# Performance work log

Hardware: AMD Instinct MI355X
Metric: run time of the kernel (lower is better)

The kernel has to match this reference:

```python
import jax, jax.numpy as jnp
import numpy as np

# Config constants (match init_kwargs / config)
B = 16        # config.BATCH_SIZE
T = 2048      # config.TRAIN_LEN
C = 256       # input channels (input_shape[-1])
K = 8         # kernel_size
F = 256       # nb_filters
DIL = 4       # dilation_rate


def setup_inputs() -> dict:
    key = jax.random.key(0)
    k1, k2, k3 = jax.random.split(key, 3)
    inputs = jax.random.normal(k1, (B, T, C), dtype=jnp.float32)
    kernel = jax.random.normal(k2, (C, K, F), dtype=jnp.float32) * 0.05
    bias = jax.random.normal(k3, (F,), dtype=jnp.float32) * 0.05
    return {"inputs": inputs, "kernel": kernel, "bias": bias}


def reference(inputs, kernel, bias):
    # Original TF layer computes, per (b,t,k,f):
    #   raw[b,t,k,f] = sum_c (x[b,t,c] * kernel[c,k,f] + bias[f])
    #               = conv[b,t,k,f] + C * bias[f]
    # (bias is added BEFORE the reduce_sum over the channel axis, so it is
    #  scaled by C — we reproduce that quirk faithfully.)
    # Then each (t,k) slice is scatter-added to output time t + k*dilation
    # (the gather_nd + zero-pad construction in TF implements exactly this
    #  dilated transposed-conv scatter; non-matching positions gather zeros),
    # and finally the last T timesteps are kept.
    Bq, Tq, Cq = inputs.shape
    Kq, Fq = kernel.shape[1], kernel.shape[2]
    conv = jnp.einsum('btc,ckf->btkf', inputs, kernel) + jnp.asarray(Cq, inputs.dtype) * bias
    L = Tq + (Kq - 1) * DIL  # final_time_len
    # scatter positions: out[i + j*DIL] += conv[:, i, j, :]
    pos = (jnp.arange(Tq)[:, None] + DIL * jnp.arange(Kq)[None, :]).reshape(-1)  # (T*K,)
    out = jnp.zeros((Bq, L, Fq), dtype=conv.dtype)
    out = out.at[:, pos, :].add(conv.reshape(Bq, Tq * Kq, Fq))
    return out[:, -Tq:, :]
```

## Files before the change

kernel.cpp:

```cpp
#include <hip/hip_runtime.h>
#include <hip/hip_bf16.h>


#define B_    16
#define T_    2048
#define C_    256
#define KT    8
#define F_    256
#define SH    28
#define BT    128
#define ROWS  (BT + SH)
#define NTASK (ROWS * 8)
#define CHW   (ROWS * 64)

typedef __attribute__((ext_vector_type(8))) short short8;
typedef __attribute__((ext_vector_type(4))) float floatx4;

__global__ __launch_bounds__(256) void wprep_kernel(const float* __restrict__ W,
                                                    ushort* __restrict__ Wf) {
    const int tid  = threadIdx.x;
    const int fid  = blockIdx.x * 4 + (tid >> 6);
    const int lane = tid & 63;
    const int g    = fid & 15;
    const int S    = fid >> 4;
    const int kh   = S & 1, j = (S >> 1) & 7, cs = S >> 4;
    const int c0   = cs * 64 + kh * 32 + (lane >> 4) * 8;
    const int f    = g * 16 + (lane & 15);
    short8 pk;
    #pragma unroll
    for (int i = 0; i < 8; ++i) {
        __hip_bfloat16 h = __float2bfloat16(W[((c0 + i) * KT + j) * F_ + f]);
        pk[i] = *reinterpret_cast<const short*>(&h);
    }
    *reinterpret_cast<short8*>(Wf + (size_t)fid * 512 + lane * 8) = pk;
}

__device__ inline short8 cvt8(float4 a, float4 b) {
    float v[8] = {a.x, a.y, a.z, a.w, b.x, b.y, b.z, b.w};
    short8 r;
    #pragma unroll
    for (int i = 0; i < 8; ++i) {
        __hip_bfloat16 h = __float2bfloat16(v[i]);
        r[i] = *reinterpret_cast<const short*>(&h);
    }
    return r;
}

__global__ __launch_bounds__(512, 2) void deconv_kernel(
        const float* __restrict__ x, const ushort* __restrict__ Wf,
        const float* __restrict__ bias, float* __restrict__ out) {
    __shared__ ushort xs[2 * CHW];
    const int t0   = blockIdx.x * BT;
    const int b    = blockIdx.y;
    const int tid  = threadIdx.x;
    const int lane = tid & 63, w = tid >> 6;
    const int wf   = w & 3, wm = w >> 2;
    const int l16  = lane & 15, q = lane >> 4;

    const int r0 = tid >> 3,          g0 = tid & 7;
    const int r1 = (tid + 512) >> 3,  g1 = tid & 7;
    const int r2 = (tid + 1024) >> 3, g2 = tid & 7;

    float4 A0, B0, A1, B1, A2, B2;

#define STAGE_LOAD(cs_) do {                                                   \
        const float4 z_ = make_float4(0.f, 0.f, 0.f, 0.f);                     \
        A0 = z_; B0 = z_; A1 = z_; B1 = z_; A2 = z_; B2 = z_;                  \
        {   const float4* p_ = reinterpret_cast<const float4*>(                \
                x + ((size_t)(b * T_ + t0 + r0) * C_ + (cs_) * 64 + g0 * 8));  \
            A0 = p_[0]; B0 = p_[1]; }                                          \
        {   const float4* p_ = reinterpret_cast<const float4*>(                \
                x + ((size_t)(b * T_ + t0 + r1) * C_ + (cs_) * 64 + g1 * 8));  \
            A1 = p_[0]; B1 = p_[1]; }                                          \
        if (tid < 224 && t0 + r2 < T_) {                                       \
            const float4* p_ = reinterpret_cast<const float4*>(                \
                x + ((size_t)(b * T_ + t0 + r2) * C_ + (cs_) * 64 + g2 * 8));  \
            A2 = p_[0]; B2 = p_[1]; } } while (0)

#define STAGE_WRITE(buf_) do {                                                 \
        ushort* d_ = xs + (buf_) * CHW;                                        \
        *reinterpret_cast<short8*>(d_ + r0 * 64 + ((g0 ^ (r0 & 7)) * 8)) =     \
            cvt8(A0, B0);                                                      \
        *reinterpret_cast<short8*>(d_ + r1 * 64 + ((g1 ^ (r1 & 7)) * 8)) =     \
            cvt8(A1, B1);                                                      \
        if (tid < 224)                                                         \
            *reinterpret_cast<short8*>(d_ + r2 * 64 + ((g2 ^ (r2 & 7)) * 8)) = \
                cvt8(A2, B2);                                                  \
        } while (0)

#define LOAD_A(buf_, s_, arr) do {                                             \
        const int j_ = (s_) >> 1, kh_ = (s_) & 1;                              \
        const int rb_ = SH - 4 * j_ + wm * 64 + l16;                           \
        _Pragma("unroll")                                                      \
        for (int mf = 0; mf < 4; ++mf) {                                       \
            const int row_ = rb_ + mf * 16;                                    \
            arr[mf] = *reinterpret_cast<const short8*>(                        \
                xs + (buf_) * CHW + row_ * 64 +                                \
                (((kh_ * 4 + q) ^ (row_ & 7)) * 8));                           \
        } } while (0)

#define LOAD_B(S_, arr) do {                                                   \
        const ushort* p_ = wbase + (size_t)(S_) * 8192;                        \
        _Pragma("unroll")                                                      \
        for (int nf = 0; nf < 4; ++nf)                                         \
            arr[nf] = *reinterpret_cast<const short8*>(p_ + nf * 512);         \
        } while (0)

#define DO_MFMA(aa, bb) do {                                                   \
        _Pragma("unroll")                                                      \
        for (int mf = 0; mf < 4; ++mf)                                         \
            _Pragma("unroll")                                                  \
            for (int nf = 0; nf < 4; ++nf)                                     \
                acc[mf][nf] = __builtin_amdgcn_mfma_f32_16x16x32_bf16(         \
                    aa[mf], bb[nf], acc[mf][nf], 0, 0, 0);                     \
        } while (0)

    const ushort* wbase = Wf + wf * 2048 + (size_t)lane * 8;

    float bf4[4];
    #pragma unroll
    for (int nf = 0; nf < 4; ++nf) bf4[nf] = bias[wf * 64 + nf * 16 + l16];

    floatx4 acc[4][4];
    #pragma unroll
    for (int mf = 0; mf < 4; ++mf)
        #pragma unroll
        for (int nf = 0; nf < 4; ++nf)
            acc[mf][nf] = (floatx4){0.f, 0.f, 0.f, 0.f};

    short8 aA[4], aB[4], bA[4], bB[4];

    STAGE_LOAD(0);
    LOAD_B(0, bA);
    LOAD_B(1, bB);
    STAGE_WRITE(0);
    __syncthreads();

    for (int cs = 0; cs < 4; ++cs) {
        const int buf = cs & 1;
        if (cs < 3) STAGE_LOAD(cs + 1);
        LOAD_A(buf, 0, aA);
        LOAD_A(buf, 1, aB);
        #pragma unroll
        for (int s = 0; s < 16; s += 2) {
            const int S = cs * 16 + s;
            __builtin_amdgcn_s_setprio(1);
            DO_MFMA(aA, bA);
            __builtin_amdgcn_s_setprio(0);
            if (s < 14) LOAD_A(buf, s + 2, aA);
            LOAD_B((S + 2) & 63, bA);
            __builtin_amdgcn_s_setprio(1);
            DO_MFMA(aB, bB);
            __builtin_amdgcn_s_setprio(0);
            if (s < 14) LOAD_A(buf, s + 3, aB);
            LOAD_B((S + 3) & 63, bB);
        }
        if (cs < 3) STAGE_WRITE(buf ^ 1);
        __syncthreads();
    }

    #pragma unroll
    for (int mf = 0; mf < 4; ++mf) {
        #pragma unroll
        for (int nf = 0; nf < 4; ++nf) {
            const int f = wf * 64 + nf * 16 + l16;
            #pragma unroll
            for (int r = 0; r < 4; ++r) {
                const int t = t0 + wm * 64 + mf * 16 + q * 4 + r;
                const int jmin = (t < T_ - SH) ? 0 : (((t - (T_ - SH)) >> 2) + 1);
                out[(size_t)(b * T_ + t) * F_ + f] =
                    acc[mf][nf][r] + (float)(8 - jmin) * 256.0f * bf4[nf];
            }
        }
    }
#undef STAGE_LOAD
#undef STAGE_WRITE
#undef LOAD_A
#undef LOAD_B
#undef DO_MFMA
}

extern "C" void kernel_launch(void* const* d_in, const int* in_sizes, int n_in,
                              void* d_out, int out_size, void* d_ws, size_t ws_size,
                              hipStream_t stream) {
    const float* x    = (const float*)d_in[0];
    const float* W    = (const float*)d_in[1];
    const float* bias = (const float*)d_in[2];
    float* out = (float*)d_out;
    ushort* Wf = (ushort*)d_ws;

    wprep_kernel<<<256, 256, 0, stream>>>(W, Wf);
    dim3 grid(T_ / BT, B_);
    deconv_kernel<<<grid, 512, 0, stream>>>(x, Wf, bias, out);
}
```

Baseline: 45.23 us.

## Switch deconv to 32x32x16 MFMA with 4 waves and 32-channel stages

```diff
diff --git a/kernel.cpp b/kernel.cpp
--- a/kernel.cpp
+++ b/kernel.cpp
@@ -10,27 +10,28 @@
 #define SH    28
 #define BT    128
 #define ROWS  (BT + SH)
-#define NTASK (ROWS * 8)
-#define CHW   (ROWS * 64)
+#define CH    32
+#define CHW   (ROWS * CH)
 
 typedef __attribute__((ext_vector_type(8))) short short8;
-typedef __attribute__((ext_vector_type(4))) float floatx4;
+typedef __attribute__((ext_vector_type(16))) float floatx16;
 
 __global__ __launch_bounds__(256) void wprep_kernel(const float* __restrict__ W,
                                                     ushort* __restrict__ Wf) {
     const int tid  = threadIdx.x;
     const int fid  = blockIdx.x * 4 + (tid >> 6);
     const int lane = tid & 63;
-    const int g    = fid & 15;
-    const int S    = fid >> 4;
-    const int kh   = S & 1, j = (S >> 1) & 7, cs = S >> 4;
-    const int c0   = cs * 64 + kh * 32 + (lane >> 4) * 8;
-    const int f    = g * 16 + (lane & 15);
+    const int l5 = lane & 31, h = lane >> 5;
+    const int nf = fid & 1, w = (fid >> 1) & 3;
+    const int S  = fid >> 3;
+    const int kh = S & 1, j = (S >> 1) & 7, cs = S >> 4;
+    const int c0 = cs * 32 + kh * 16 + h * 8;
+    const int f  = w * 64 + nf * 32 + l5;
     short8 pk;
     #pragma unroll
     for (int i = 0; i < 8; ++i) {
-        __hip_bfloat16 h = __float2bfloat16(W[((c0 + i) * KT + j) * F_ + f]);
-        pk[i] = *reinterpret_cast<const short*>(&h);
+        __hip_bfloat16 v = __float2bfloat16(W[((c0 + i) * KT + j) * F_ + f]);
+        pk[i] = *reinterpret_cast<const short*>(&v);
     }
     *reinterpret_cast<short8*>(Wf + (size_t)fid * 512 + lane * 8) = pk;
 }
@@ -40,13 +41,13 @@
     short8 r;
     #pragma unroll
     for (int i = 0; i < 8; ++i) {
-        __hip_bfloat16 h = __float2bfloat16(v[i]);
-        r[i] = *reinterpret_cast<const short*>(&h);
+        __hip_bfloat16 t = __float2bfloat16(v[i]);
+        r[i] = *reinterpret_cast<const short*>(&t);
     }
     return r;
 }
 
-__global__ __launch_bounds__(512, 2) void deconv_kernel(
+__global__ __launch_bounds__(256, 1) void deconv_kernel(
         const float* __restrict__ x, const ushort* __restrict__ Wf,
         const float* __restrict__ bias, float* __restrict__ out) {
     __shared__ ushort xs[2 * CHW];
@@ -54,81 +55,79 @@
     const int b    = blockIdx.y;
     const int tid  = threadIdx.x;
     const int lane = tid & 63, w = tid >> 6;
-    const int wf   = w & 3, wm = w >> 2;
-    const int l16  = lane & 15, q = lane >> 4;
+    const int l5   = lane & 31, h = lane >> 5;
 
-    const int r0 = tid >> 3,          g0 = tid & 7;
-    const int r1 = (tid + 512) >> 3,  g1 = tid & 7;
-    const int r2 = (tid + 1024) >> 3, g2 = tid & 7;
+    const int r0 = tid >> 2,            g0 = tid & 3;
+    const int r1 = (tid + 256) >> 2,    g1 = tid & 3;
+    const int r2 = (tid + 512) >> 2,    g2 = tid & 3;
 
     float4 A0, B0, A1, B1, A2, B2;
 
 #define STAGE_LOAD(cs_) do {                                                   \
         const float4 z_ = make_float4(0.f, 0.f, 0.f, 0.f);                     \
-        A0 = z_; B0 = z_; A1 = z_; B1 = z_; A2 = z_; B2 = z_;                  \
+        A2 = z_; B2 = z_;                                                      \
         {   const float4* p_ = reinterpret_cast<const float4*>(                \
-                x + ((size_t)(b * T_ + t0 + r0) * C_ + (cs_) * 64 + g0 * 8));  \
+                x + ((size_t)(b * T_ + t0 + r0) * C_ + (cs_) * CH + g0 * 8));  \
             A0 = p_[0]; B0 = p_[1]; }                                          \
         {   const float4* p_ = reinterpret_cast<const float4*>(                \
-                x + ((size_t)(b * T_ + t0 + r1) * C_ + (cs_) * 64 + g1 * 8));  \
+                x + ((size_t)(b * T_ + t0 + r1) * C_ + (cs_) * CH + g1 * 8));  \
             A1 = p_[0]; B1 = p_[1]; }                                          \
-        if (tid < 224 && t0 + r2 < T_) {                                       \
+        if (tid < 112 && t0 + r2 < T_) {                                       \
             const float4* p_ = reinterpret_cast<const float4*>(                \
-                x + ((size_t)(b * T_ + t0 + r2) * C_ + (cs_) * 64 + g2 * 8));  \
+                x + ((size_t)(b * T_ + t0 + r2) * C_ + (cs_) * CH + g2 * 8));  \
             A2 = p_[0]; B2 = p_[1]; } } while (0)
 
 #define STAGE_WRITE(buf_) do {                                                 \
         ushort* d_ = xs + (buf_) * CHW;                                        \
-        *reinterpret_cast<short8*>(d_ + r0 * 64 + ((g0 ^ (r0 & 7)) * 8)) =     \
-            cvt8(A0, B0);                                                      \
-        *reinterpret_cast<short8*>(d_ + r1 * 64 + ((g1 ^ (r1 & 7)) * 8)) =     \
-            cvt8(A1, B1);                                                      \
-        if (tid < 224)                                                         \
-            *reinterpret_cast<short8*>(d_ + r2 * 64 + ((g2 ^ (r2 & 7)) * 8)) = \
-                cvt8(A2, B2);                                                  \
+        *reinterpret_cast<short8*>(d_ + r0 * CH +                              \
+            (((g0 ^ r0 ^ (r0 >> 2)) & 3) * 8)) = cvt8(A0, B0);                 \
+        *reinterpret_cast<short8*>(d_ + r1 * CH +                              \
+            (((g1 ^ r1 ^ (r1 >> 2)) & 3) * 8)) = cvt8(A1, B1);                 \
+        if (tid < 112)                                                         \
+            *reinterpret_cast<short8*>(d_ + r2 * CH +                          \
+                (((g2 ^ r2 ^ (r2 >> 2)) & 3) * 8)) = cvt8(A2, B2);             \
         } while (0)
 
-#define LOAD_A(buf_, s_, arr) do {                                             \
-        const int j_ = (s_) >> 1, kh_ = (s_) & 1;                              \
-        const int rb_ = SH - 4 * j_ + wm * 64 + l16;                           \
+#define LOAD_A(buf_, j_, kh_, arr) do {                                        \
+        const int rb_ = SH - 4 * (j_) + l5;                                    \
         _Pragma("unroll")                                                      \
         for (int mf = 0; mf < 4; ++mf) {                                       \
-            const int row_ = rb_ + mf * 16;                                    \
+            const int row_ = rb_ + mf * 32;                                    \
+            const int sl_  = (((kh_) * 2 + h) ^ row_ ^ (row_ >> 2)) & 3;       \
             arr[mf] = *reinterpret_cast<const short8*>(                        \
-                xs + (buf_) * CHW + row_ * 64 +                                \
-                (((kh_ * 4 + q) ^ (row_ & 7)) * 8));                           \
+                xs + (buf_) * CHW + row_ * CH + sl_ * 8);                      \
         } } while (0)
 
 #define LOAD_B(S_, arr) do {                                                   \
-        const ushort* p_ = wbase + (size_t)(S_) * 8192;                        \
-        _Pragma("unroll")                                                      \
-        for (int nf = 0; nf < 4; ++nf)                                         \
-            arr[nf] = *reinterpret_cast<const short8*>(p_ + nf * 512);         \
+        const ushort* p_ = wbase + (size_t)(S_) * 4096;                        \
+        arr[0] = *reinterpret_cast<const short8*>(p_);                         \
+        arr[1] = *reinterpret_cast<const short8*>(p_ + 512);                   \
         } while (0)
 
 #define DO_MFMA(aa, bb) do {                                                   \
         _Pragma("unroll")                                                      \
-        for (int mf = 0; mf < 4; ++mf)                                         \
-            _Pragma("unroll")                                                  \
-            for (int nf = 0; nf < 4; ++nf)                                     \
-                acc[mf][nf] = __builtin_amdgcn_mfma_f32_16x16x32_bf16(         \
-                    aa[mf], bb[nf], acc[mf][nf], 0, 0, 0);                     \
-        } while (0)
+        for (int mf = 0; mf < 4; ++mf) {                                       \
+            acc[mf][0] = __builtin_amdgcn_mfma_f32_32x32x16_bf16(              \
+                aa[mf], bb[0], acc[mf][0], 0, 0, 0);                           \
+            acc[mf][1] = __builtin_amdgcn_mfma_f32_32x32x16_bf16(              \
+                aa[mf], bb[1], acc[mf][1], 0, 0, 0);                           \
+        } } while (0)
 
-    const ushort* wbase = Wf + wf * 2048 + (size_t)lane * 8;
+    const ushort* wbase = Wf + (size_t)(w * 2) * 512 + lane * 8;
 
-    float bf4[4];
-    #pragma unroll
-    for (int nf = 0; nf < 4; ++nf) bf4[nf] = bias[wf * 64 + nf * 16 + l16];
+    float bf2[2];
+    bf2[0] = bias[w * 64 + l5];
+    bf2[1] = bias[w * 64 + 32 + l5];
 
-    floatx4 acc[4][4];
+    floatx16 acc[4][2];
     #pragma unroll
     for (int mf = 0; mf < 4; ++mf)
         #pragma unroll
-        for (int nf = 0; nf < 4; ++nf)
-            acc[mf][nf] = (floatx4){0.f, 0.f, 0.f, 0.f};
+        for (int nf = 0; nf < 2; ++nf)
+            #pragma unroll
+            for (int r = 0; r < 16; ++r) acc[mf][nf][r] = 0.f;
 
-    short8 aA[4], aB[4], bA[4], bB[4];
+    short8 aA[4], aB[4], bA[2], bB[2];
 
     STAGE_LOAD(0);
     LOAD_B(0, bA);
@@ -136,40 +135,36 @@
     STAGE_WRITE(0);
     __syncthreads();
 
-    for (int cs = 0; cs < 4; ++cs) {
+    for (int cs = 0; cs < 8; ++cs) {
         const int buf = cs & 1;
-        if (cs < 3) STAGE_LOAD(cs + 1);
-        LOAD_A(buf, 0, aA);
-        LOAD_A(buf, 1, aB);
+        if (cs < 7) STAGE_LOAD(cs + 1);
+        LOAD_A(buf, 0, 0, aA);
+        LOAD_A(buf, 0, 1, aB);
         #pragma unroll
         for (int s = 0; s < 16; s += 2) {
-            const int S = cs * 16 + s;
-            __builtin_amdgcn_s_setprio(1);
             DO_MFMA(aA, bA);
-            __builtin_amdgcn_s_setprio(0);
-            if (s < 14) LOAD_A(buf, s + 2, aA);
-            LOAD_B((S + 2) & 63, bA);
-            __builtin_amdgcn_s_setprio(1);
+            if (s < 14) LOAD_A(buf, (s + 2) >> 1, 0, aA);
+            LOAD_B((cs * 16 + s + 2) & 127, bA);
             DO_MFMA(aB, bB);
-            __builtin_amdgcn_s_setprio(0);
-            if (s < 14) LOAD_A(buf, s + 3, aB);
-            LOAD_B((S + 3) & 63, bB);
+            if (s < 14) LOAD_A(buf, (s + 3) >> 1, 1, aB);
+            LOAD_B((cs * 16 + s + 3) & 127, bB);
         }
-        if (cs < 3) STAGE_WRITE(buf ^ 1);
+        if (cs < 7) STAGE_WRITE(buf ^ 1);
         __syncthreads();
     }
 
     #pragma unroll
     for (int mf = 0; mf < 4; ++mf) {
         #pragma unroll
-        for (int nf = 0; nf < 4; ++nf) {
-            const int f = wf * 64 + nf * 16 + l16;
+        for (int nf = 0; nf < 2; ++nf) {
+            const int f = w * 64 + nf * 32 + l5;
             #pragma unroll
-            for (int r = 0; r < 4; ++r) {
-                const int t = t0 + wm * 64 + mf * 16 + q * 4 + r;
+            for (int r = 0; r < 16; ++r) {
+                const int rowin = (r & 3) + 8 * (r >> 2) + 4 * h;
+                const int t = t0 + mf * 32 + rowin;
                 const int jmin = (t < T_ - SH) ? 0 : (((t - (T_ - SH)) >> 2) + 1);
                 out[(size_t)(b * T_ + t) * F_ + f] =
-                    acc[mf][nf][r] + (float)(8 - jmin) * 256.0f * bf4[nf];
+                    acc[mf][nf][r] + (float)(8 - jmin) * 256.0f * bf2[nf];
             }
         }
     }
@@ -191,5 +186,5 @@
 
     wprep_kernel<<<256, 256, 0, stream>>>(W, Wf);
     dim3 grid(T_ / BT, B_);
-    deconv_kernel<<<grid, 512, 0, stream>>>(x, Wf, bias, out);
+    deconv_kernel<<<grid, 256, 0, stream>>>(x, Wf, bias, out);
 }
```

Measured after the change: 60.34 us. 33.4% more time.
